# Kernel optimization log

Hardware: AMD Instinct MI355X
Metric: run time of the kernel (lower is better)

Reference implementation:

```python
import jax, jax.numpy as jnp
import numpy as np

B, S, H, NH = 4, 2048, 1024, 16
D = H // NH

def setup_inputs() -> dict:
    key = jax.random.key(0)
    ks = jax.random.split(key, 9)
    sc = 1.0 / np.sqrt(H)
    return {
        "x": jax.random.normal(ks[0], (B, S, H), jnp.float32),
        "Wq": jax.random.normal(ks[1], (H, H), jnp.float32) * sc,
        "bq": jax.random.normal(ks[2], (H,), jnp.float32) * 0.01,
        "Wk": jax.random.normal(ks[3], (H, H), jnp.float32) * sc,
        "bk": jax.random.normal(ks[4], (H,), jnp.float32) * 0.01,
        "Wv": jax.random.normal(ks[5], (H, H), jnp.float32) * sc,
        "bv": jax.random.normal(ks[6], (H,), jnp.float32) * 0.01,
        "Wo": jax.random.normal(ks[7], (H, H), jnp.float32) * sc,
        "bo": jax.random.normal(ks[8], (H,), jnp.float32) * 0.01,
    }

def reference(x, Wq, bq, Wk, bk, Wv, bv, Wo, bo):
    # torch Linear: y = x @ W.T + b
    def proj(x, W, b):
        # [B,S,H] -> [B,NH,S,D]
        y = jnp.einsum('bsh,oh->bso', x, W) + b
        return y.reshape(B, S, NH, D).transpose(0, 2, 1, 3)
    q = proj(x, Wq, bq)
    k = proj(x, Wk, bk)
    v = proj(x, Wv, bv)
    scores = jnp.einsum('bhqd,bhkd->bhqk', q, k) / jnp.sqrt(jnp.float32(D))
    p = jax.nn.softmax(scores, axis=-1)  # [B,NH,S,S]
    o = jnp.einsum('bhqk,bhkd->bhqd', p, v)  # dropout p=0 (eval)
    o = o.transpose(0, 2, 1, 3).reshape(B, S, H)
    return jnp.einsum('bsh,oh->bso', o, Wo) + bo
```

## Files before the change

### kernel.cpp

```cpp
#include <hip/hip_runtime.h>


#define DEV __device__ __forceinline__

typedef __bf16 bf16x8 __attribute__((ext_vector_type(8)));
typedef __bf16 bf16x4 __attribute__((ext_vector_type(4)));
typedef float floatx4 __attribute__((ext_vector_type(4)));

constexpr int Bdim = 4, SS = 2048, HH = 1024, NHH = 16, DD = 64;
constexpr int MM = Bdim * SS;

DEV void async16(const void* g, void* l) {
  __builtin_amdgcn_global_load_lds(
      (const __attribute__((address_space(1))) unsigned int*)g,
      (__attribute__((address_space(3))) unsigned int*)l, 16, 0, 0);
}

DEV int swz2(int r) { return (r ^ (r >> 2)) & 3; }
DEV int swz3(int r) { return (r ^ (r >> 3)) & 7; }

__global__ __launch_bounds__(256) void cast_bf16_kernel(
    const float* __restrict__ x, const float* __restrict__ wq,
    const float* __restrict__ wk, const float* __restrict__ wv,
    const float* __restrict__ wo,
    __bf16* __restrict__ xb, __bf16* __restrict__ wqb, __bf16* __restrict__ wkb,
    __bf16* __restrict__ wvb, __bf16* __restrict__ wob) {
  const float* src; __bf16* dst; int n4;
  switch (blockIdx.z) {
    case 0: src = x;  dst = xb;  n4 = MM * HH / 4; break;
    case 1: src = wq; dst = wqb; n4 = HH * HH / 4; break;
    case 2: src = wk; dst = wkb; n4 = HH * HH / 4; break;
    case 3: src = wv; dst = wvb; n4 = HH * HH / 4; break;
    default: src = wo; dst = wob; n4 = HH * HH / 4; break;
  }
  int stride = gridDim.x * blockDim.x;
  for (int i = blockIdx.x * blockDim.x + threadIdx.x; i < n4; i += stride) {
    float4 v = ((const float4*)src)[i];
    bf16x4 o;
    o[0] = (__bf16)v.x; o[1] = (__bf16)v.y; o[2] = (__bf16)v.z; o[3] = (__bf16)v.w;
    ((bf16x4*)dst)[i] = o;
  }
}

__global__ __launch_bounds__(256, 3) void proj_qkv_kernel(
    const __bf16* __restrict__ xb,
    const __bf16* __restrict__ wqb, const __bf16* __restrict__ wkb,
    const __bf16* __restrict__ wvb,
    const float* __restrict__ bq, const float* __restrict__ bk,
    const float* __restrict__ bv,
    __bf16* __restrict__ Q, __bf16* __restrict__ Kc, __bf16* __restrict__ Vt) {
  __shared__ __align__(16) __bf16 As[2][128 * 32];
  __shared__ __align__(16) __bf16 Bs[2][3][64 * 32];

  const int lid = blockIdx.x;
  const int xcd = lid & 7, slot = lid >> 3;
  const int mp = xcd + 8 * (slot >> 4);
  const int np = slot & 15;
  const int m0 = mp * 128, n0 = np * 64;

  const int t = threadIdx.x;
  const int lane = t & 63, quad = lane >> 4, l16 = lane & 15;
  const int wid = t >> 6;

  const __bf16* const Wm[3] = {wqb, wkb, wvb};

  const int srow = t >> 2, sc = t & 3;
  const __bf16* Ag0 = xb + (size_t)(m0 + srow) * HH + (sc ^ swz2(srow)) * 8;
  const __bf16* Ag1 = xb + (size_t)(m0 + srow + 64) * HH + (sc ^ swz2(srow + 64)) * 8;
  const __bf16* Bg[3];
#pragma unroll
  for (int mo = 0; mo < 3; ++mo)
    Bg[mo] = Wm[mo] + (size_t)(n0 + srow) * HH + (sc ^ swz2(srow)) * 8;

  int aoff[2], boff[4];
#pragma unroll
  for (int mi = 0; mi < 2; ++mi) {
    int ra = wid * 32 + mi * 16 + l16;
    aoff[mi] = ra * 32 + (quad ^ swz2(ra)) * 8;
  }
#pragma unroll
  for (int ni = 0; ni < 4; ++ni) {
    int rb = ni * 16 + l16;
    boff[ni] = rb * 32 + (quad ^ swz2(rb)) * 8;
  }

  floatx4 acc[3][2][4] = {};

  async16(Ag0, &As[0][t * 8]);
  async16(Ag1, &As[0][2048 + t * 8]);
#pragma unroll
  for (int mo = 0; mo < 3; ++mo) async16(Bg[mo], &Bs[0][mo][t * 8]);

  for (int it = 0; it < HH / 32; ++it) {
    const int cur = it & 1;
    __syncthreads();

    if (it + 1 < HH / 32) {
      const int k = (it + 1) * 32;
      const int nxt = cur ^ 1;
      async16(Ag0 + k, &As[nxt][t * 8]);
      async16(Ag1 + k, &As[nxt][2048 + t * 8]);
#pragma unroll
      for (int mo = 0; mo < 3; ++mo) async16(Bg[mo] + k, &Bs[nxt][mo][t * 8]);
    }

    bf16x8 af[2];
#pragma unroll
    for (int mi = 0; mi < 2; ++mi) af[mi] = *(const bf16x8*)&As[cur][aoff[mi]];
#pragma unroll
    for (int mo = 0; mo < 3; ++mo) {
      bf16x8 bfr[4];
#pragma unroll
      for (int ni = 0; ni < 4; ++ni) bfr[ni] = *(const bf16x8*)&Bs[cur][mo][boff[ni]];
#pragma unroll
      for (int mi = 0; mi < 2; ++mi)
#pragma unroll
        for (int ni = 0; ni < 4; ++ni)
          acc[mo][mi][ni] = __builtin_amdgcn_mfma_f32_16x16x32_bf16(
              af[mi], bfr[ni], acc[mo][mi][ni], 0, 0, 0);
    }
  }

  const float qscale = 0.125f * 1.44269504088896f;
#pragma unroll
  for (int mo = 0; mo < 3; ++mo) {
    const float* bias = mo == 0 ? bq : mo == 1 ? bk : bv;
#pragma unroll
    for (int ni = 0; ni < 4; ++ni) {
      int n = n0 + ni * 16 + l16;
      float bval = bias[n];
      int h = n >> 6, d = n & 63;
#pragma unroll
      for (int mi = 0; mi < 2; ++mi) {
        int mbase = m0 + wid * 32 + mi * 16 + quad * 4;
        int bb = mbase >> 11, sbase = mbase & (SS - 1);
        size_t bh = (size_t)(bb * NHH + h);
        if (mo == 2) {
          bf16x4 pv;
#pragma unroll
          for (int r = 0; r < 4; ++r) pv[r] = (__bf16)(acc[mo][mi][ni][r] + bval);
          *(bf16x4*)&Vt[(bh * DD + d) * SS + sbase] = pv;
        } else {
#pragma unroll
          for (int r = 0; r < 4; ++r) {
            float v = acc[mo][mi][ni][r] + bval;
            if (mo == 0) Q [(bh * SS + sbase + r) * DD + d] = (__bf16)(v * qscale);
            else         Kc[(bh * SS + sbase + r) * DD + d] = (__bf16)v;
          }
        }
      }
    }
  }
}

DEV void gemm_db128(const __bf16* __restrict__ Ablk, const __bf16* __restrict__ Bblk,
                    __bf16* As, __bf16* Bs, floatx4 acc[4][4]) {
  const int t = threadIdx.x;
  const int lane = t & 63, quad = lane >> 4, l16 = lane & 15;
  const int wid = t >> 6;
  const int wm = (wid >> 1) * 64, wn = (wid & 1) * 64;

  const int srow = t >> 2, sc = t & 3;
  const __bf16* Ag0 = Ablk + (size_t)srow * HH + (sc ^ swz2(srow)) * 8;
  const __bf16* Ag1 = Ablk + (size_t)(srow + 64) * HH + (sc ^ swz2(srow + 64)) * 8;
  const __bf16* Bg0 = Bblk + (size_t)srow * HH + (sc ^ swz2(srow)) * 8;
  const __bf16* Bg1 = Bblk + (size_t)(srow + 64) * HH + (sc ^ swz2(srow + 64)) * 8;

  int aoff[4], boff[4];
#pragma unroll
  for (int i = 0; i < 4; ++i) {
    int ra = wm + i * 16 + l16;
    aoff[i] = ra * 32 + (quad ^ swz2(ra)) * 8;
    int rb = wn + i * 16 + l16;
    boff[i] = rb * 32 + (quad ^ swz2(rb)) * 8;
  }

  async16(Ag0, As + t * 8);
  async16(Ag1, As + 2048 + t * 8);
  async16(Bg0, Bs + t * 8);
  async16(Bg1, Bs + 2048 + t * 8);

  for (int it = 0; it < HH / 32; ++it) {
    const int cur = it & 1;
    __syncthreads();

    if (it + 1 < HH / 32) {
      const int k = (it + 1) * 32;
      const int nxt = (cur ^ 1) * 4096;
      async16(Ag0 + k, As + nxt + t * 8);
      async16(Ag1 + k, As + nxt + 2048 + t * 8);
      async16(Bg0 + k, Bs + nxt + t * 8);
      async16(Bg1 + k, Bs + nxt + 2048 + t * 8);
    }

    bf16x8 af[4], bfr[4];
#pragma unroll
    for (int i = 0; i < 4; ++i) {
      af[i]  = *(const bf16x8*)&As[cur * 4096 + aoff[i]];
      bfr[i] = *(const bf16x8*)&Bs[cur * 4096 + boff[i]];
    }
#pragma unroll
    for (int mi = 0; mi < 4; ++mi)
#pragma unroll
      for (int ni = 0; ni < 4; ++ni)
        acc[mi][ni] = __builtin_amdgcn_mfma_f32_16x16x32_bf16(af[mi], bfr[ni],
                                                              acc[mi][ni], 0, 0, 0);
  }
}

__global__ __launch_bounds__(256) void proj_out_kernel(
    const __bf16* __restrict__ Ob, const __bf16* __restrict__ wob,
    const float* __restrict__ bo, float* __restrict__ out) {
  __shared__ __align__(16) __bf16 As[2 * 128 * 32];
  __shared__ __align__(16) __bf16 Bs[2 * 128 * 32];
  const int lid = blockIdx.x;
  const int xcd = lid & 7, slot = lid >> 3;
  const int mp = xcd + 8 * (slot >> 3);
  const int np = slot & 7;
  const int m0 = mp * 128, n0 = np * 128;
  floatx4 acc[4][4] = {};
  gemm_db128(Ob + (size_t)m0 * HH, wob + (size_t)n0 * HH, As, Bs, acc);
  const int t = threadIdx.x, lane = t & 63, quad = lane >> 4, l16 = lane & 15;
  const int wid = t >> 6, wm = (wid >> 1) * 64, wn = (wid & 1) * 64;
#pragma unroll
  for (int ni = 0; ni < 4; ++ni) {
    int n = n0 + wn + ni * 16 + l16;
    float bval = bo[n];
#pragma unroll
    for (int mi = 0; mi < 4; ++mi)
#pragma unroll
      for (int r = 0; r < 4; ++r) {
        int m = m0 + wm + mi * 16 + quad * 4 + r;
        out[(size_t)m * HH + n] = acc[mi][ni][r] + bval;
      }
  }
}

__global__ __launch_bounds__(256, 2) void attn_kernel(
    const __bf16* __restrict__ Q, const __bf16* __restrict__ Kc,
    const __bf16* __restrict__ Vt, __bf16* __restrict__ Ob) {
  __shared__ __align__(16) __bf16 Ks[2][64 * 64];
  __shared__ __align__(16) __bf16 Vs[2][64 * 64];
  __shared__ __align__(16) __bf16 Ps[4 * 64 * 40];

  const int t = threadIdx.x, lane = t & 63, quad = lane >> 4, l16 = lane & 15;
  const int wid = t >> 6;
  const int L = blockIdx.x;
  const int qt = L >> 6, bhx = L & 63;
  const int b = bhx >> 4, h = bhx & 15;
  const size_t bh = (size_t)b * NHH + h;
  const __bf16* Qg = Q + (bh * SS + (size_t)qt * 256) * DD;
  const __bf16* Kg = Kc + bh * SS * DD;
  const __bf16* Vg = Vt + bh * DD * SS;

  const int srow = t >> 3;
  const int sc = t & 7;

  const __bf16* KgA = Kg + (size_t)srow * DD + (sc ^ swz3(srow)) * 8;
  const __bf16* KgB = Kg + (size_t)(srow + 32) * DD + (sc ^ swz3(srow + 32)) * 8;
  const __bf16* VgA = Vg + (size_t)srow * SS + (sc ^ swz3(srow)) * 8;
  const __bf16* VgB = Vg + (size_t)(srow + 32) * SS + (sc ^ swz3(srow + 32)) * 8;

  bf16x8 qf[4][2];
#pragma unroll
  for (int ni = 0; ni < 4; ++ni)
#pragma unroll
    for (int ks = 0; ks < 2; ++ks)
      qf[ni][ks] = *(const bf16x8*)(Qg + (size_t)(wid * 64 + ni * 16 + l16) * DD
                                    + (ks * 4 + quad) * 8);

  floatx4 oacc[4][4] = {};
  float rsum[4] = {0.f, 0.f, 0.f, 0.f};

  __bf16* Pw = Ps + wid * (64 * 40);

  int koff[4][2];
#pragma unroll
  for (int mi = 0; mi < 4; ++mi) {
    int r = mi * 16 + l16;
#pragma unroll
    for (int ks = 0; ks < 2; ++ks)
      koff[mi][ks] = r * 64 + ((ks * 4 + quad) ^ swz3(r)) * 8;
  }

  async16(KgA, &Ks[0][t * 8]);
  async16(KgB, &Ks[0][2048 + t * 8]);
  async16(VgA, &Vs[0][t * 8]);
  async16(VgB, &Vs[0][2048 + t * 8]);

  for (int kt = 0; kt < SS / 64; ++kt) {
    const int cur = kt & 1;
    __syncthreads();

    if (kt + 1 < SS / 64) {
      const int kk = (kt + 1) * 64;
      const int nxt = cur ^ 1;
      async16(KgA + (size_t)kk * DD, &Ks[nxt][t * 8]);
      async16(KgB + (size_t)kk * DD, &Ks[nxt][2048 + t * 8]);
      async16(VgA + kk, &Vs[nxt][t * 8]);
      async16(VgB + kk, &Vs[nxt][2048 + t * 8]);
    }

    floatx4 sacc[4][4];
#pragma unroll
    for (int mi = 0; mi < 4; ++mi)
#pragma unroll
      for (int ni = 0; ni < 4; ++ni) sacc[mi][ni] = floatx4{0.f, 0.f, 0.f, 0.f};
#pragma unroll
    for (int ks = 0; ks < 2; ++ks) {
      bf16x8 kf[4];
#pragma unroll
      for (int mi = 0; mi < 4; ++mi) kf[mi] = *(const bf16x8*)&Ks[cur][koff[mi][ks]];
#pragma unroll
      for (int mi = 0; mi < 4; ++mi)
#pragma unroll
        for (int ni = 0; ni < 4; ++ni)
          sacc[mi][ni] = __builtin_amdgcn_mfma_f32_16x16x32_bf16(kf[mi], qf[ni][ks],
                                                                 sacc[mi][ni], 0, 0, 0);
    }

#pragma unroll
    for (int hf = 0; hf < 2; ++hf) {
#pragma unroll
      for (int mh = 0; mh < 2; ++mh) {
        const int mi = hf * 2 + mh;
#pragma unroll
        for (int ni = 0; ni < 4; ++ni) {
          bf16x4 pk;
#pragma unroll
          for (int r = 0; r < 4; ++r) {
            float p = __builtin_amdgcn_exp2f(sacc[mi][ni][r]);
            rsum[ni] += p;
            pk[r] = (__bf16)p;
          }
          *(bf16x4*)&Pw[(ni * 16 + l16) * 40 + mh * 16 + quad * 4] = pk;
        }
      }
      bf16x8 ap[4], bv8[4];
#pragma unroll
      for (int mq = 0; mq < 4; ++mq)
        ap[mq] = *(const bf16x8*)&Pw[(mq * 16 + l16) * 40 + quad * 8];
#pragma unroll
      for (int nj = 0; nj < 4; ++nj) bv8[nj] = *(const bf16x8*)&Vs[cur][koff[nj][hf]];
#pragma unroll
      for (int mq = 0; mq < 4; ++mq)
#pragma unroll
        for (int nj = 0; nj < 4; ++nj)
          oacc[mq][nj] = __builtin_amdgcn_mfma_f32_16x16x32_bf16(ap[mq], bv8[nj],
                                                                 oacc[mq][nj], 0, 0, 0);
    }
  }

#pragma unroll
  for (int ni = 0; ni < 4; ++ni) {
    rsum[ni] += __shfl_xor(rsum[ni], 16, 64);
    rsum[ni] += __shfl_xor(rsum[ni], 32, 64);
  }

  const int s0 = qt * 256 + wid * 64;
#pragma unroll
  for (int mq = 0; mq < 4; ++mq) {
#pragma unroll
    for (int r = 0; r < 4; ++r) {
      float inv = 1.f / __shfl(rsum[mq], quad * 4 + r, 64);
      int s = s0 + mq * 16 + quad * 4 + r;
#pragma unroll
      for (int nj = 0; nj < 4; ++nj) {
        int d = nj * 16 + l16;
        Ob[((size_t)b * SS + s) * HH + h * DD + d] = (__bf16)(oacc[mq][nj][r] * inv);
      }
    }
  }
}

extern "C" void kernel_launch(void* const* d_in, const int* in_sizes, int n_in,
                              void* d_out, int out_size, void* d_ws, size_t ws_size,
                              hipStream_t stream) {
  const float* x  = (const float*)d_in[0];
  const float* Wq = (const float*)d_in[1];
  const float* bq = (const float*)d_in[2];
  const float* Wk = (const float*)d_in[3];
  const float* bk = (const float*)d_in[4];
  const float* Wv = (const float*)d_in[5];
  const float* bv = (const float*)d_in[6];
  const float* Wo = (const float*)d_in[7];
  const float* bo = (const float*)d_in[8];
  float* out = (float*)d_out;

  char* ws = (char*)d_ws;
  __bf16* xb  = (__bf16*)(ws);
  __bf16* wqb = (__bf16*)(ws + 16777216);
  __bf16* wkb = (__bf16*)(ws + 18874368);
  __bf16* wvb = (__bf16*)(ws + 20971520);
  __bf16* wob = (__bf16*)(ws + 23068672);
  __bf16* Qb  = (__bf16*)(ws + 25165824);
  __bf16* Kb  = (__bf16*)(ws + 41943040);
  __bf16* Vtb = (__bf16*)(ws + 58720256);
  __bf16* Ob  = (__bf16*)(ws + 75497472);

  cast_bf16_kernel<<<dim3(256, 1, 5), 256, 0, stream>>>(x, Wq, Wk, Wv, Wo,
                                                        xb, wqb, wkb, wvb, wob);
  proj_qkv_kernel<<<dim3(1024), 256, 0, stream>>>(xb, wqb, wkb, wvb,
                                                  bq, bk, bv, Qb, Kb, Vtb);
  attn_kernel<<<dim3(512), 256, 0, stream>>>(Qb, Kb, Vtb, Ob);
  proj_out_kernel<<<dim3(512), 256, 0, stream>>>(Ob, wob, bo, out);
}
```

Measured before the change: 285.3 us.

## Build P operand in registers with permlane16 swap instead of LDS round trip

The attention kernel no longer writes the exponentiated score tile P to shared memory and reads it back as the MFMA A-operand. It packs P values to bf16 pairs in registers, uses v_permlane16_swap to exchange halves between lane groups, and compensates by permuting the V-fragment column offsets (voff with swapped quad order). This removes the per-wave LDS stores, loads and the Ps buffer, which also reduces LDS footprint. The risk is correctness of the lane/k-index permutation and the dependence on the gfx950 permlane16_swap instruction.

```diff
diff --git a/kernel.cpp b/kernel.cpp
--- a/kernel.cpp
+++ b/kernel.cpp
@@ -5,7 +5,9 @@
 
 typedef __bf16 bf16x8 __attribute__((ext_vector_type(8)));
 typedef __bf16 bf16x4 __attribute__((ext_vector_type(4)));
+typedef __bf16 bf16x2 __attribute__((ext_vector_type(2)));
 typedef float floatx4 __attribute__((ext_vector_type(4)));
+typedef unsigned int uintx4 __attribute__((ext_vector_type(4)));
 
 constexpr int Bdim = 4, SS = 2048, HH = 1024, NHH = 16, DD = 64;
 constexpr int MM = Bdim * SS;
@@ -18,6 +20,17 @@
 
 DEV int swz2(int r) { return (r ^ (r >> 2)) & 3; }
 DEV int swz3(int r) { return (r ^ (r >> 3)) & 7; }
+
+DEV unsigned pkbf16(float lo, float hi) {
+  bf16x2 t;
+  t[0] = (__bf16)lo;
+  t[1] = (__bf16)hi;
+  return __builtin_bit_cast(unsigned, t);
+}
+
+DEV void pswap16(unsigned& a, unsigned& b) {
+  asm("v_permlane16_swap_b32 %0, %1" : "+v"(a), "+v"(b));
+}
 
 __global__ __launch_bounds__(256) void cast_bf16_kernel(
     const float* __restrict__ x, const float* __restrict__ wq,
@@ -241,7 +254,6 @@
     const __bf16* __restrict__ Vt, __bf16* __restrict__ Ob) {
   __shared__ __align__(16) __bf16 Ks[2][64 * 64];
   __shared__ __align__(16) __bf16 Vs[2][64 * 64];
-  __shared__ __align__(16) __bf16 Ps[4 * 64 * 40];
 
   const int t = threadIdx.x, lane = t & 63, quad = lane >> 4, l16 = lane & 15;
   const int wid = t >> 6;
@@ -272,8 +284,6 @@
   floatx4 oacc[4][4] = {};
   float rsum[4] = {0.f, 0.f, 0.f, 0.f};
 
-  __bf16* Pw = Ps + wid * (64 * 40);
-
   int koff[4][2];
 #pragma unroll
   for (int mi = 0; mi < 4; ++mi) {
@@ -281,6 +291,15 @@
 #pragma unroll
     for (int ks = 0; ks < 2; ++ks)
       koff[mi][ks] = r * 64 + ((ks * 4 + quad) ^ swz3(r)) * 8;
+  }
+  const int sq = ((quad & 1) << 1) | (quad >> 1);
+  int voff[4][2];
+#pragma unroll
+  for (int nj = 0; nj < 4; ++nj) {
+    int r = nj * 16 + l16;
+#pragma unroll
+    for (int hf = 0; hf < 2; ++hf)
+      voff[nj][hf] = r * 64 + ((hf * 4 + sq) ^ swz3(r)) * 8;
   }
 
   async16(KgA, &Ks[0][t * 8]);
@@ -321,27 +340,29 @@
 
 #pragma unroll
     for (int hf = 0; hf < 2; ++hf) {
-#pragma unroll
-      for (int mh = 0; mh < 2; ++mh) {
-        const int mi = hf * 2 + mh;
-#pragma unroll
-        for (int ni = 0; ni < 4; ++ni) {
-          bf16x4 pk;
+      bf16x8 ap[4], bv8[4];
+#pragma unroll
+      for (int mq = 0; mq < 4; ++mq) {
+        float p[2][4];
+#pragma unroll
+        for (int m = 0; m < 2; ++m)
 #pragma unroll
           for (int r = 0; r < 4; ++r) {
-            float p = __builtin_amdgcn_exp2f(sacc[mi][ni][r]);
-            rsum[ni] += p;
-            pk[r] = (__bf16)p;
+            float e = __builtin_amdgcn_exp2f(sacc[hf * 2 + m][mq][r]);
+            rsum[mq] += e;
+            p[m][r] = e;
           }
-          *(bf16x4*)&Pw[(ni * 16 + l16) * 40 + mh * 16 + quad * 4] = pk;
-        }
+        unsigned x0 = pkbf16(p[0][0], p[0][1]);
+        unsigned x1 = pkbf16(p[0][2], p[0][3]);
+        unsigned y0 = pkbf16(p[1][0], p[1][1]);
+        unsigned y1 = pkbf16(p[1][2], p[1][3]);
+        pswap16(x0, y0);
+        pswap16(x1, y1);
+        uintx4 u = {x0, x1, y0, y1};
+        ap[mq] = __builtin_bit_cast(bf16x8, u);
       }
-      bf16x8 ap[4], bv8[4];
-#pragma unroll
-      for (int mq = 0; mq < 4; ++mq)
-        ap[mq] = *(const bf16x8*)&Pw[(mq * 16 + l16) * 40 + quad * 8];
-#pragma unroll
-      for (int nj = 0; nj < 4; ++nj) bv8[nj] = *(const bf16x8*)&Vs[cur][koff[nj][hf]];
+#pragma unroll
+      for (int nj = 0; nj < 4; ++nj) bv8[nj] = *(const bf16x8*)&Vs[cur][voff[nj][hf]];
 #pragma unroll
       for (int mq = 0; mq < 4; ++mq)
 #pragma unroll
```

Measured after the change: 277.6 us. -2.7%, faster.
